# Performance work log

Hardware: AMD Instinct MI355X
Metric: run time of the kernel (lower is better)

Reference implementation:

```python
import jax, jax.numpy as jnp
import numpy as np

N_USERS = 100000
N_ITEMS = 50000
N_NODES = N_USERS + N_ITEMS  # 150000
N_EDGES = 1000000
N_INTENTS = 4
EMBED_K = 64
CHUNK = EMBED_K // N_INTENTS  # 16
N_LAYERS = 3


def setup_inputs() -> dict:
    key = jax.random.key(0)
    k1, k2, k3, k4 = jax.random.split(key, 4)
    Gu = jax.random.normal(k1, (N_USERS, EMBED_K), dtype=jnp.float32) * 0.1
    Gi = jax.random.normal(k2, (N_ITEMS, EMBED_K), dtype=jnp.float32) * 0.1
    edge_index = jax.random.randint(k3, (2, N_EDGES), 0, N_NODES, dtype=jnp.int64)
    edge_index_intents = jax.random.normal(k4, (N_INTENTS, N_EDGES), dtype=jnp.float32)
    return {"Gu": Gu, "Gi": Gi, "edge_index": edge_index,
            "edge_index_intents": edge_index_intents}


def dgcf_layer(x, row, col, edge_index_intents):
    # x: [N, K, C]; edge_index_intents: [K, E]
    w = jax.nn.softmax(edge_index_intents, axis=0).T  # [E, K]
    deg = (jax.ops.segment_sum(w, row, num_segments=N_NODES)
           + jax.ops.segment_sum(w, col, num_segments=N_NODES))  # [N, K]
    # deg^-0.5 with inf -> 0 (as in the torch code)
    dis = jnp.where(deg > 0, 1.0 / jnp.sqrt(jnp.maximum(deg, 1e-12)), 0.0)  # [N, K]
    norm = dis[row] * dis[col]  # [E, K]
    msg = norm[:, :, None] * x[row]  # [E, K, C] gather-multiply
    return jax.ops.segment_sum(msg, col, num_segments=N_NODES)  # scatter-add at targets


def reference(Gu, Gi, edge_index, edge_index_intents):
    row, col = edge_index[0], edge_index[1]
    # ego embeddings split into intent chunks: [N, K, C]
    x = jnp.concatenate([Gu, Gi], axis=0).reshape(N_NODES, N_INTENTS, CHUNK)
    for _ in range(N_LAYERS):
        x = dgcf_layer(x, row, col, edge_index_intents)
    return x
```

## Files before the change

kernel.cpp:

```cpp
#include <hip/hip_runtime.h>
#include <hip/hip_bf16.h>
#include <hip/hip_fp16.h>
#include <math.h>

#define N_USERS 100000
#define N_ITEMS 50000
#define N_NODES 150000
#define N_EDGES 1000000
#define N_GU_FLAT (N_USERS * 64)
#define N_ALL_FLAT (N_NODES * 64)
#define NBUCK 586
#define HPITCH (2 * NBUCK)
#define EPB 4096
#define NEB ((N_EDGES + EPB - 1) / EPB)
#define BCAP 2048
#define FIXS 16777216.0f

typedef __hip_bfloat16 bf16;
typedef unsigned short ushort_t;
typedef unsigned int uint_t;
typedef unsigned long long u64_t;

__device__ __forceinline__ ushort_t f2bs(float f) {
    bf16 h = __float2bfloat16(f);
    return *reinterpret_cast<ushort_t*>(&h);
}
__device__ __forceinline__ float lo2f(uint_t u) {
    float f; *reinterpret_cast<uint_t*>(&f) = u << 16; return f;
}
__device__ __forceinline__ float hi2f(uint_t u) {
    float f; *reinterpret_cast<uint_t*>(&f) = u & 0xFFFF0000u; return f;
}
__device__ __forceinline__ uint_t pack2(float a, float b) {
    return (uint_t)f2bs(a) | ((uint_t)f2bs(b) << 16);
}
__device__ __forceinline__ ushort_t f2hs(float f) {
    __half h = __float2half(f);
    return *reinterpret_cast<ushort_t*>(&h);
}
__device__ __forceinline__ float hs2f(ushort_t u) {
    __half h; *reinterpret_cast<ushort_t*>(&h) = u;
    return __half2float(h);
}
__device__ __forceinline__ int fix24(float w) {
    return (int)__float2int_rn(w * FIXS);
}

__global__ __launch_bounds__(1024) void s1_hist_cast(
        const int* __restrict__ ei,
        const float* __restrict__ Gu, const float* __restrict__ Gi,
        ushort_t* __restrict__ xG, uint_t* __restrict__ H, int gE) {
    int b = blockIdx.x;
    int t = threadIdx.x;
    if (b >= gE) {
        long base = ((long)(b - gE) * 1024 + t) * 4;
        if (base >= N_ALL_FLAT) return;
        float4 v = (base < N_GU_FLAT) ? *(const float4*)(Gu + base)
                                      : *(const float4*)(Gi + (base - N_GU_FLAT));
        uint2 o;
        o.x = pack2(v.x, v.y);
        o.y = pack2(v.z, v.w);
        *(uint2*)(xG + base) = o;
        return;
    }
    __shared__ uint_t h[HPITCH];
    for (int j = t; j < HPITCH; j += 1024) h[j] = 0;
    __syncthreads();
    int eb = b * EPB;
    int lim = min(EPB, N_EDGES - eb);
    for (int i = t; i < lim; i += 1024) {
        int e = eb + i;
        int r = ei[e];
        int c = ei[N_EDGES + e];
        atomicAdd(&h[c >> 8], 1u);
        atomicAdd(&h[NBUCK + (r >> 8)], 1u);
    }
    __syncthreads();
    for (int j = t; j < HPITCH; j += 1024) H[(size_t)b * HPITCH + j] = h[j];
}

__global__ __launch_bounds__(256) void s2a_scan_blocks(
        const uint_t* __restrict__ H, uint_t* __restrict__ bases,
        uint_t* __restrict__ totals) {
    int j = blockIdx.x;
    int t = threadIdx.x;
    __shared__ uint_t s[256];
    uint_t v = (t < NEB) ? H[(size_t)t * HPITCH + j] : 0u;
    s[t] = v;
    __syncthreads();
    for (int off = 1; off < 256; off <<= 1) {
        uint_t a = (t >= off) ? s[t - off] : 0u;
        __syncthreads();
        s[t] += a;
        __syncthreads();
    }
    if (t < NEB) bases[(size_t)t * HPITCH + j] = s[t] - v;
    if (t == 255) totals[j] = s[255];
}

__global__ __launch_bounds__(1024) void s2b_bucket_scan(
        const uint_t* __restrict__ totals,
        uint_t* __restrict__ col_base, uint_t* __restrict__ row_base) {
    __shared__ uint_t s[1024];
    int t = threadIdx.x;
    uint_t v = (t < NBUCK) ? totals[t] : 0u;
    s[t] = v;
    __syncthreads();
    for (int off = 1; off < 1024; off <<= 1) {
        uint_t a = (t >= off) ? s[t - off] : 0u;
        __syncthreads();
        s[t] += a;
        __syncthreads();
    }
    if (t < NBUCK) col_base[t] = s[t] - v;
    if (t == NBUCK - 1) col_base[NBUCK] = s[t];
    __syncthreads();
    uint_t w = (t < NBUCK) ? totals[NBUCK + t] : 0u;
    s[t] = w;
    __syncthreads();
    for (int off = 1; off < 1024; off <<= 1) {
        uint_t a = (t >= off) ? s[t - off] : 0u;
        __syncthreads();
        s[t] += a;
        __syncthreads();
    }
    if (t < NBUCK) row_base[t] = s[t] - w;
    if (t == NBUCK - 1) row_base[NBUCK] = s[t];
}

__global__ __launch_bounds__(1024) void s3_scatter(
        const int* __restrict__ ei, const float* __restrict__ intents,
        const uint_t* __restrict__ bases,
        const uint_t* __restrict__ col_base, const uint_t* __restrict__ row_base,
        uint_t* __restrict__ tmp_meta, u64_t* __restrict__ tmp_w,
        u64_t* __restrict__ tmp_row) {
    extern __shared__ char smem[];
    u64_t*  cw    = (u64_t*)smem;
    u64_t*  rw    = (u64_t*)(smem + 32768);
    uint_t* cmeta = (uint_t*)(smem + 65536);
    uint_t* cpos  = (uint_t*)(smem + 81920);
    uint_t* rpos  = (uint_t*)(smem + 98304);
    uint_t* ctr   = (uint_t*)(smem + 114688);
    uint_t* lexcl = (uint_t*)(smem + 119376);
    uint_t* stmp  = (uint_t*)(smem + 124064);
    int b = blockIdx.x, t = threadIdx.x;
    for (int j = t; j < HPITCH; j += 1024) ctr[j] = 0;
    __syncthreads();
    int eb = b * EPB;
    int lim = min(EPB, N_EDGES - eb);
    int  jcol[4], jrow[4];
    uint_t rkc[4], rkr[4], meta[4];
    u64_t cwv[4], rwv[4];
    bool val[4];
#pragma unroll
    for (int q = 0; q < 4; ++q) {
        int i = t + q * 1024;
        val[q] = (i < lim);
        int e = eb + (val[q] ? i : 0);
        int r = ei[e];
        int c = ei[N_EDGES + e];
        float v0 = intents[e];
        float v1 = intents[N_EDGES + e];
        float v2 = intents[2 * N_EDGES + e];
        float v3 = intents[3 * N_EDGES + e];
        float m  = fmaxf(fmaxf(v0, v1), fmaxf(v2, v3));
        float x0 = __expf(v0 - m), x1 = __expf(v1 - m);
        float x2 = __expf(v2 - m), x3 = __expf(v3 - m);
        float inv = 1.0f / (x0 + x1 + x2 + x3);
        float w0 = x0 * inv, w1 = x1 * inv, w2 = x2 * inv, w3 = x3 * inv;
        jcol[q] = c >> 8;
        jrow[q] = r >> 8;
        if (val[q]) {
            rkc[q] = atomicAdd(&ctr[jcol[q]], 1u);
            rkr[q] = atomicAdd(&ctr[NBUCK + jrow[q]], 1u);
        }
        meta[q] = ((uint_t)(c & 255) << 24) | (uint_t)r;
        cwv[q]  = (u64_t)pack2(w0, w1) | ((u64_t)pack2(w2, w3) << 32);
        rwv[q]  = (u64_t)f2hs(w0) | ((u64_t)f2hs(w1) << 16) |
                  ((u64_t)f2hs(w2) << 32) | ((u64_t)(uint_t)(r & 255) << 48);
    }
    __syncthreads();
    {
        uint_t v = (t < NBUCK) ? ctr[t] : 0u;
        stmp[t] = v;
        __syncthreads();
        for (int off = 1; off < 1024; off <<= 1) {
            uint_t a = (t >= off) ? stmp[t - off] : 0u;
            __syncthreads();
            stmp[t] += a;
            __syncthreads();
        }
        if (t < NBUCK) lexcl[t] = stmp[t] - v;
    }
    __syncthreads();
    {
        uint_t v = (t < NBUCK) ? ctr[NBUCK + t] : 0u;
        stmp[t] = v;
        __syncthreads();
        for (int off = 1; off < 1024; off <<= 1) {
            uint_t a = (t >= off) ? stmp[t - off] : 0u;
            __syncthreads();
            stmp[t] += a;
            __syncthreads();
        }
        if (t < NBUCK) lexcl[NBUCK + t] = stmp[t] - v;
    }
    __syncthreads();
#pragma unroll
    for (int q = 0; q < 4; ++q) {
        if (!val[q]) continue;
        uint_t lp = lexcl[jcol[q]] + rkc[q];
        cmeta[lp] = meta[q];
        cw[lp]    = cwv[q];
        cpos[lp]  = col_base[jcol[q]] + bases[(size_t)b * HPITCH + jcol[q]] + rkc[q];
        uint_t lr = lexcl[NBUCK + jrow[q]] + rkr[q];
        rw[lr]    = rwv[q];
        rpos[lr]  = row_base[jrow[q]] + bases[(size_t)b * HPITCH + NBUCK + jrow[q]] + rkr[q];
    }
    __syncthreads();
    for (int i = t; i < lim; i += 1024) {
        uint_t p = cpos[i];
        tmp_meta[p] = cmeta[i];
        tmp_w[p]    = cw[i];
        tmp_row[rpos[i]] = rw[i];
    }
}

__global__ __launch_bounds__(1024) void s4_finalize(
        const uint_t* __restrict__ tmp_meta, const u64_t* __restrict__ tmp_w,
        const u64_t* __restrict__ tmp_row,
        const uint_t* __restrict__ col_base, const uint_t* __restrict__ row_base,
        uint_t* __restrict__ rec_src, int* __restrict__ offs_c, int* __restrict__ cnt_c,
        float* __restrict__ dis) {
    __shared__ uint_t meta_s[BCAP];
    __shared__ u64_t  w_s[BCAP];
    __shared__ u64_t  rw_s[BCAP];
    __shared__ uint_t hist[256], excl[256], run[256], sc[256];
    __shared__ int deg[1024];
    int b = blockIdx.x, t = threadIdx.x;
    if (t < 256) { hist[t] = 0u; run[t] = 0u; }
    deg[t] = 0;
    __syncthreads();
    uint_t c0 = col_base[b];
    int nc = min((int)(col_base[b + 1] - c0), BCAP);
    uint_t r0 = row_base[b];
    int nr = min((int)(row_base[b + 1] - r0), BCAP);
    for (int i = t; i < nc; i += 1024) {
        meta_s[i] = tmp_meta[c0 + i];
        w_s[i]    = tmp_w[c0 + i];
    }
    for (int i = t; i < nr; i += 1024) rw_s[i] = tmp_row[r0 + i];
    __syncthreads();
    for (int i = t; i < nc; i += 1024) {
        uint_t nl = meta_s[i] >> 24;
        u64_t w = w_s[i];
        atomicAdd(&hist[nl], 1u);
        atomicAdd(&deg[nl * 4 + 0], fix24(lo2f((uint_t)w)));
        atomicAdd(&deg[nl * 4 + 1], fix24(hi2f((uint_t)w)));
        atomicAdd(&deg[nl * 4 + 2], fix24(lo2f((uint_t)(w >> 32))));
        atomicAdd(&deg[nl * 4 + 3], fix24(hi2f((uint_t)(w >> 32))));
    }
    for (int i = t; i < nr; i += 1024) {
        u64_t rv = rw_s[i];
        uint_t nl = (uint_t)(rv >> 48) & 255u;
        float w0 = hs2f((ushort_t)(rv & 0xFFFF));
        float w1 = hs2f((ushort_t)((rv >> 16) & 0xFFFF));
        float w2 = hs2f((ushort_t)((rv >> 32) & 0xFFFF));
        float w3 = 1.0f - w0 - w1 - w2;
        atomicAdd(&deg[nl * 4 + 0], fix24(w0));
        atomicAdd(&deg[nl * 4 + 1], fix24(w1));
        atomicAdd(&deg[nl * 4 + 2], fix24(w2));
        atomicAdd(&deg[nl * 4 + 3], fix24(w3));
    }
    __syncthreads();
    if (t < 256) sc[t] = hist[t];
    __syncthreads();
    for (int off = 1; off < 256; off <<= 1) {
        uint_t a = (t < 256 && t >= off) ? sc[t - off] : 0u;
        __syncthreads();
        if (t < 256) sc[t] += a;
        __syncthreads();
    }
    if (t < 256) excl[t] = sc[t] - hist[t];
    __syncthreads();
    for (int i = t; i < nc; i += 1024) {
        uint_t m = meta_s[i];
        uint_t nl = m >> 24;
        uint_t p = atomicAdd(&run[nl], 1u);
        rec_src[c0 + excl[nl] + p] = m & 0x00FFFFFFu;
    }
    if (t < 256) {
        int n = b * 256 + t;
        if (n < N_NODES) {
            offs_c[n] = (int)(c0 + excl[t]);
            cnt_c[n]  = (int)hist[t];
            float d0 = (float)deg[t * 4 + 0] * (1.0f / FIXS);
            float d1 = (float)deg[t * 4 + 1] * (1.0f / FIXS);
            float d2 = (float)deg[t * 4 + 2] * (1.0f / FIXS);
            float d3 = (float)deg[t * 4 + 3] * (1.0f / FIXS);
            float4 dd;
            dd.x = (d0 > 0.f) ? rsqrtf(fmaxf(d0, 1e-12f)) : 0.f;
            dd.y = (d1 > 0.f) ? rsqrtf(fmaxf(d1, 1e-12f)) : 0.f;
            dd.z = (d2 > 0.f) ? rsqrtf(fmaxf(d2, 1e-12f)) : 0.f;
            dd.w = (d3 > 0.f) ? rsqrtf(fmaxf(d3, 1e-12f)) : 0.f;
            *(float4*)(dis + (size_t)n * 4) = dd;
        }
    }
}

template <int MODE>
__global__ __launch_bounds__(256) void dg_agg(const ushort_t* __restrict__ xin,
                                              ushort_t* __restrict__ xout_b,
                                              float* __restrict__ xout_f,
                                              const uint_t* __restrict__ rec_src,
                                              const int* __restrict__ cnt_c,
                                              const int* __restrict__ offs_c,
                                              const float* __restrict__ dis) {
    int n = (blockIdx.x * 256 + threadIdx.x) >> 3;
    if (n >= N_NODES) return;
    int j = threadIdx.x & 7, k = j >> 1;
    int base = offs_c[n];
    int cnt  = cnt_c[n];
    float dd = dis[n * 4 + k];
    float a0 = 0.f, a1 = 0.f, a2 = 0.f, a3 = 0.f;
    float a4 = 0.f, a5 = 0.f, a6 = 0.f, a7 = 0.f;
    int i = 0;
    for (; i + 2 <= cnt; i += 2) {
        int s0 = (int)rec_src[base + i];
        int s1 = (int)rec_src[base + i + 1];
        uint4 x0 = *(const uint4*)(xin + (long)s0 * 64 + j * 8);
        uint4 x1 = *(const uint4*)(xin + (long)s1 * 64 + j * 8);
        float n0 = 1.f, n1 = 1.f;
        if (MODE == 0) { n0 = dis[s0 * 4 + k]; n1 = dis[s1 * 4 + k]; }
        a0 = fmaf(n0, lo2f(x0.x), a0); a1 = fmaf(n0, hi2f(x0.x), a1);
        a2 = fmaf(n0, lo2f(x0.y), a2); a3 = fmaf(n0, hi2f(x0.y), a3);
        a4 = fmaf(n0, lo2f(x0.z), a4); a5 = fmaf(n0, hi2f(x0.z), a5);
        a6 = fmaf(n0, lo2f(x0.w), a6); a7 = fmaf(n0, hi2f(x0.w), a7);
        a0 = fmaf(n1, lo2f(x1.x), a0); a1 = fmaf(n1, hi2f(x1.x), a1);
        a2 = fmaf(n1, lo2f(x1.y), a2); a3 = fmaf(n1, hi2f(x1.y), a3);
        a4 = fmaf(n1, lo2f(x1.z), a4); a5 = fmaf(n1, hi2f(x1.z), a5);
        a6 = fmaf(n1, lo2f(x1.w), a6); a7 = fmaf(n1, hi2f(x1.w), a7);
    }
    if (i < cnt) {
        int s0 = (int)rec_src[base + i];
        uint4 x0 = *(const uint4*)(xin + (long)s0 * 64 + j * 8);
        float n0 = (MODE == 0) ? dis[s0 * 4 + k] : 1.f;
        a0 = fmaf(n0, lo2f(x0.x), a0); a1 = fmaf(n0, hi2f(x0.x), a1);
        a2 = fmaf(n0, lo2f(x0.y), a2); a3 = fmaf(n0, hi2f(x0.y), a3);
        a4 = fmaf(n0, lo2f(x0.z), a4); a5 = fmaf(n0, hi2f(x0.z), a5);
        a6 = fmaf(n0, lo2f(x0.w), a6); a7 = fmaf(n0, hi2f(x0.w), a7);
    }
    float sc = (MODE == 2) ? dd : dd * dd;
    a0 *= sc; a1 *= sc; a2 *= sc; a3 *= sc;
    a4 *= sc; a5 *= sc; a6 *= sc; a7 *= sc;
    long o = (long)n * 64 + j * 8;
    if (MODE == 2) {
        *(float4*)(xout_f + o)     = make_float4(a0, a1, a2, a3);
        *(float4*)(xout_f + o + 4) = make_float4(a4, a5, a6, a7);
    } else {
        uint4 ob;
        ob.x = pack2(a0, a1); ob.y = pack2(a2, a3);
        ob.z = pack2(a4, a5); ob.w = pack2(a6, a7);
        *(uint4*)(xout_b + o) = ob;
    }
}

extern "C" void kernel_launch(void* const* d_in, const int* in_sizes, int n_in,
                              void* d_out, int out_size, void* d_ws, size_t ws_size,
                              hipStream_t stream) {
    const float* Gu      = (const float*)d_in[0];
    const float* Gi      = (const float*)d_in[1];
    const int*   ei      = (const int*)d_in[2];
    const float* intents = (const float*)d_in[3];
    float* out = (float*)d_out;

    char* ws = (char*)d_ws;
    size_t off = 0;
    int* offs_c = (int*)(ws + off);       off += (size_t)N_NODES * 4;
    int* cnt_c  = (int*)(ws + off);       off += (size_t)N_NODES * 4;
    float* dis  = (float*)(ws + off);     off += (size_t)N_NODES * 16;
    uint_t* rec_src = (uint_t*)(ws + off); off += (size_t)N_EDGES * 4;
    uint_t* col_base = (uint_t*)(ws + off); off += 4096;
    uint_t* row_base = (uint_t*)(ws + off); off += 4096;
    uint_t* totals   = (uint_t*)(ws + off); off += 8192;
    ushort_t* xG = (ushort_t*)(ws + off); off += (size_t)N_ALL_FLAT * 2;
    ushort_t* xA = (ushort_t*)(ws + off); off += (size_t)N_ALL_FLAT * 2;
    ushort_t* xB = (ushort_t*)(ws + off); off += (size_t)N_ALL_FLAT * 2;
    uint_t* tmp_meta = (uint_t*)xA;
    u64_t*  tmp_w    = (u64_t*)((char*)xA + 4000000);
    u64_t*  tmp_row  = (u64_t*)xB;
    uint_t* H     = (uint_t*)((char*)xB + 8000000);
    uint_t* bases = (uint_t*)((char*)xB + 9200000);
    (void)ws_size; (void)in_sizes; (void)n_in; (void)out_size;

    const int gE1 = NEB;
    const int gC1 = (N_ALL_FLAT / 4 + 1023) / 1024;

    s1_hist_cast<<<gE1 + gC1, 1024, 0, stream>>>(ei, Gu, Gi, xG, H, gE1);
    s2a_scan_blocks<<<HPITCH, 256, 0, stream>>>(H, bases, totals);
    s2b_bucket_scan<<<1, 1024, 0, stream>>>(totals, col_base, row_base);

    const size_t S3_LDS = 128160;
    hipFuncSetAttribute((const void*)s3_scatter,
                        hipFuncAttributeMaxDynamicSharedMemorySize, (int)S3_LDS);
    s3_scatter<<<NEB, 1024, S3_LDS, stream>>>(ei, intents, bases, col_base, row_base,
                                              tmp_meta, tmp_w, tmp_row);
    s4_finalize<<<NBUCK, 1024, 0, stream>>>(tmp_meta, tmp_w, tmp_row,
                                            col_base, row_base,
                                            rec_src, offs_c, cnt_c, dis);

    int gAgg = (N_NODES * 8 + 255) / 256;
    dg_agg<0><<<gAgg, 256, 0, stream>>>(xG, xA, nullptr, rec_src, cnt_c, offs_c, dis);
    dg_agg<1><<<gAgg, 256, 0, stream>>>(xA, xB, nullptr, rec_src, cnt_c, offs_c, dis);
    dg_agg<2><<<gAgg, 256, 0, stream>>>(xB, nullptr, out, rec_src, cnt_c, offs_c, dis);
}
```

Measured before the change: 232.3 us.

## Use fixed-capacity bucket slots and cooperative index loading in aggregation

```diff
diff --git a/kernel.cpp b/kernel.cpp
--- a/kernel.cpp
+++ b/kernel.cpp
@@ -79,7 +79,7 @@
     for (int j = t; j < HPITCH; j += 1024) H[(size_t)b * HPITCH + j] = h[j];
 }
 
-__global__ __launch_bounds__(256) void s2a_scan_blocks(
+__global__ __launch_bounds__(256) void s2_scan_blocks(
         const uint_t* __restrict__ H, uint_t* __restrict__ bases,
         uint_t* __restrict__ totals) {
     int j = blockIdx.x;
@@ -98,40 +98,9 @@
     if (t == 255) totals[j] = s[255];
 }
 
-__global__ __launch_bounds__(1024) void s2b_bucket_scan(
-        const uint_t* __restrict__ totals,
-        uint_t* __restrict__ col_base, uint_t* __restrict__ row_base) {
-    __shared__ uint_t s[1024];
-    int t = threadIdx.x;
-    uint_t v = (t < NBUCK) ? totals[t] : 0u;
-    s[t] = v;
-    __syncthreads();
-    for (int off = 1; off < 1024; off <<= 1) {
-        uint_t a = (t >= off) ? s[t - off] : 0u;
-        __syncthreads();
-        s[t] += a;
-        __syncthreads();
-    }
-    if (t < NBUCK) col_base[t] = s[t] - v;
-    if (t == NBUCK - 1) col_base[NBUCK] = s[t];
-    __syncthreads();
-    uint_t w = (t < NBUCK) ? totals[NBUCK + t] : 0u;
-    s[t] = w;
-    __syncthreads();
-    for (int off = 1; off < 1024; off <<= 1) {
-        uint_t a = (t >= off) ? s[t - off] : 0u;
-        __syncthreads();
-        s[t] += a;
-        __syncthreads();
-    }
-    if (t < NBUCK) row_base[t] = s[t] - w;
-    if (t == NBUCK - 1) row_base[NBUCK] = s[t];
-}
-
 __global__ __launch_bounds__(1024) void s3_scatter(
         const int* __restrict__ ei, const float* __restrict__ intents,
         const uint_t* __restrict__ bases,
-        const uint_t* __restrict__ col_base, const uint_t* __restrict__ row_base,
         uint_t* __restrict__ tmp_meta, u64_t* __restrict__ tmp_w,
         u64_t* __restrict__ tmp_row) {
     extern __shared__ char smem[];
@@ -212,10 +181,10 @@
         uint_t lp = lexcl[jcol[q]] + rkc[q];
         cmeta[lp] = meta[q];
         cw[lp]    = cwv[q];
-        cpos[lp]  = col_base[jcol[q]] + bases[(size_t)b * HPITCH + jcol[q]] + rkc[q];
+        cpos[lp]  = (uint_t)jcol[q] * BCAP + bases[(size_t)b * HPITCH + jcol[q]] + rkc[q];
         uint_t lr = lexcl[NBUCK + jrow[q]] + rkr[q];
         rw[lr]    = rwv[q];
-        rpos[lr]  = row_base[jrow[q]] + bases[(size_t)b * HPITCH + NBUCK + jrow[q]] + rkr[q];
+        rpos[lr]  = (uint_t)jrow[q] * BCAP + bases[(size_t)b * HPITCH + NBUCK + jrow[q]] + rkr[q];
     }
     __syncthreads();
     for (int i = t; i < lim; i += 1024) {
@@ -228,8 +197,7 @@
 
 __global__ __launch_bounds__(1024) void s4_finalize(
         const uint_t* __restrict__ tmp_meta, const u64_t* __restrict__ tmp_w,
-        const u64_t* __restrict__ tmp_row,
-        const uint_t* __restrict__ col_base, const uint_t* __restrict__ row_base,
+        const u64_t* __restrict__ tmp_row, const uint_t* __restrict__ totals,
         uint_t* __restrict__ rec_src, int* __restrict__ offs_c, int* __restrict__ cnt_c,
         float* __restrict__ dis) {
     __shared__ uint_t meta_s[BCAP];
@@ -241,15 +209,14 @@
     if (t < 256) { hist[t] = 0u; run[t] = 0u; }
     deg[t] = 0;
     __syncthreads();
-    uint_t c0 = col_base[b];
-    int nc = min((int)(col_base[b + 1] - c0), BCAP);
-    uint_t r0 = row_base[b];
-    int nr = min((int)(row_base[b + 1] - r0), BCAP);
+    uint_t c0 = (uint_t)b * BCAP;
+    int nc = min((int)totals[b], BCAP);
+    int nr = min((int)totals[NBUCK + b], BCAP);
     for (int i = t; i < nc; i += 1024) {
         meta_s[i] = tmp_meta[c0 + i];
         w_s[i]    = tmp_w[c0 + i];
     }
-    for (int i = t; i < nr; i += 1024) rw_s[i] = tmp_row[r0 + i];
+    for (int i = t; i < nr; i += 1024) rw_s[i] = tmp_row[c0 + i];
     __syncthreads();
     for (int i = t; i < nc; i += 1024) {
         uint_t nl = meta_s[i] >> 24;
@@ -318,37 +285,31 @@
                                               const float* __restrict__ dis) {
     int n = (blockIdx.x * 256 + threadIdx.x) >> 3;
     if (n >= N_NODES) return;
-    int j = threadIdx.x & 7, k = j >> 1;
+    int lane = threadIdx.x & 63;
+    int j = lane & 7, k = j >> 1;
+    int sg = lane & 56;
     int base = offs_c[n];
     int cnt  = cnt_c[n];
     float dd = dis[n * 4 + k];
     float a0 = 0.f, a1 = 0.f, a2 = 0.f, a3 = 0.f;
     float a4 = 0.f, a5 = 0.f, a6 = 0.f, a7 = 0.f;
-    int i = 0;
-    for (; i + 2 <= cnt; i += 2) {
-        int s0 = (int)rec_src[base + i];
-        int s1 = (int)rec_src[base + i + 1];
-        uint4 x0 = *(const uint4*)(xin + (long)s0 * 64 + j * 8);
-        uint4 x1 = *(const uint4*)(xin + (long)s1 * 64 + j * 8);
-        float n0 = 1.f, n1 = 1.f;
-        if (MODE == 0) { n0 = dis[s0 * 4 + k]; n1 = dis[s1 * 4 + k]; }
-        a0 = fmaf(n0, lo2f(x0.x), a0); a1 = fmaf(n0, hi2f(x0.x), a1);
-        a2 = fmaf(n0, lo2f(x0.y), a2); a3 = fmaf(n0, hi2f(x0.y), a3);
-        a4 = fmaf(n0, lo2f(x0.z), a4); a5 = fmaf(n0, hi2f(x0.z), a5);
-        a6 = fmaf(n0, lo2f(x0.w), a6); a7 = fmaf(n0, hi2f(x0.w), a7);
-        a0 = fmaf(n1, lo2f(x1.x), a0); a1 = fmaf(n1, hi2f(x1.x), a1);
-        a2 = fmaf(n1, lo2f(x1.y), a2); a3 = fmaf(n1, hi2f(x1.y), a3);
-        a4 = fmaf(n1, lo2f(x1.z), a4); a5 = fmaf(n1, hi2f(x1.z), a5);
-        a6 = fmaf(n1, lo2f(x1.w), a6); a7 = fmaf(n1, hi2f(x1.w), a7);
-    }
-    if (i < cnt) {
-        int s0 = (int)rec_src[base + i];
-        uint4 x0 = *(const uint4*)(xin + (long)s0 * 64 + j * 8);
-        float n0 = (MODE == 0) ? dis[s0 * 4 + k] : 1.f;
-        a0 = fmaf(n0, lo2f(x0.x), a0); a1 = fmaf(n0, hi2f(x0.x), a1);
-        a2 = fmaf(n0, lo2f(x0.y), a2); a3 = fmaf(n0, hi2f(x0.y), a3);
-        a4 = fmaf(n0, lo2f(x0.z), a4); a5 = fmaf(n0, hi2f(x0.z), a5);
-        a6 = fmaf(n0, lo2f(x0.w), a6); a7 = fmaf(n0, hi2f(x0.w), a7);
+    for (int c = 0; c < cnt; c += 8) {
+        int idx = c + j;
+        uint_t sv = (idx < cnt) ? rec_src[base + idx] : 0u;
+        int srcs[8];
+#pragma unroll
+        for (int i = 0; i < 8; ++i) srcs[i] = (int)__shfl(sv, sg + i, 64);
+#pragma unroll
+        for (int i = 0; i < 8; ++i) {
+            bool v = (c + i) < cnt;
+            int src = v ? srcs[i] : srcs[0];
+            float nk = v ? ((MODE == 0) ? dis[src * 4 + k] : 1.f) : 0.f;
+            uint4 xu = *(const uint4*)(xin + (long)src * 64 + j * 8);
+            a0 = fmaf(nk, lo2f(xu.x), a0); a1 = fmaf(nk, hi2f(xu.x), a1);
+            a2 = fmaf(nk, lo2f(xu.y), a2); a3 = fmaf(nk, hi2f(xu.y), a3);
+            a4 = fmaf(nk, lo2f(xu.z), a4); a5 = fmaf(nk, hi2f(xu.z), a5);
+            a6 = fmaf(nk, lo2f(xu.w), a6); a7 = fmaf(nk, hi2f(xu.w), a7);
+        }
     }
     float sc = (MODE == 2) ? dd : dd * dd;
     a0 *= sc; a1 *= sc; a2 *= sc; a3 *= sc;
@@ -379,34 +340,30 @@
     int* offs_c = (int*)(ws + off);       off += (size_t)N_NODES * 4;
     int* cnt_c  = (int*)(ws + off);       off += (size_t)N_NODES * 4;
     float* dis  = (float*)(ws + off);     off += (size_t)N_NODES * 16;
-    uint_t* rec_src = (uint_t*)(ws + off); off += (size_t)N_EDGES * 4;
-    uint_t* col_base = (uint_t*)(ws + off); off += 4096;
-    uint_t* row_base = (uint_t*)(ws + off); off += 4096;
+    uint_t* rec_src = (uint_t*)(ws + off); off += (size_t)NBUCK * BCAP * 4;
     uint_t* totals   = (uint_t*)(ws + off); off += 8192;
     ushort_t* xG = (ushort_t*)(ws + off); off += (size_t)N_ALL_FLAT * 2;
     ushort_t* xA = (ushort_t*)(ws + off); off += (size_t)N_ALL_FLAT * 2;
     ushort_t* xB = (ushort_t*)(ws + off); off += (size_t)N_ALL_FLAT * 2;
     uint_t* tmp_meta = (uint_t*)xA;
-    u64_t*  tmp_w    = (u64_t*)((char*)xA + 4000000);
+    u64_t*  tmp_w    = (u64_t*)((char*)xA + (size_t)NBUCK * BCAP * 4);
     u64_t*  tmp_row  = (u64_t*)xB;
-    uint_t* H     = (uint_t*)((char*)xB + 8000000);
-    uint_t* bases = (uint_t*)((char*)xB + 9200000);
+    uint_t* H     = (uint_t*)((char*)xB + (size_t)NBUCK * BCAP * 8);
+    uint_t* bases = (uint_t*)((char*)xB + (size_t)NBUCK * BCAP * 8 + 1200000);
     (void)ws_size; (void)in_sizes; (void)n_in; (void)out_size;
 
     const int gE1 = NEB;
     const int gC1 = (N_ALL_FLAT / 4 + 1023) / 1024;
 
     s1_hist_cast<<<gE1 + gC1, 1024, 0, stream>>>(ei, Gu, Gi, xG, H, gE1);
-    s2a_scan_blocks<<<HPITCH, 256, 0, stream>>>(H, bases, totals);
-    s2b_bucket_scan<<<1, 1024, 0, stream>>>(totals, col_base, row_base);
+    s2_scan_blocks<<<HPITCH, 256, 0, stream>>>(H, bases, totals);
 
     const size_t S3_LDS = 128160;
     hipFuncSetAttribute((const void*)s3_scatter,
                         hipFuncAttributeMaxDynamicSharedMemorySize, (int)S3_LDS);
-    s3_scatter<<<NEB, 1024, S3_LDS, stream>>>(ei, intents, bases, col_base, row_base,
+    s3_scatter<<<NEB, 1024, S3_LDS, stream>>>(ei, intents, bases,
                                               tmp_meta, tmp_w, tmp_row);
-    s4_finalize<<<NBUCK, 1024, 0, stream>>>(tmp_meta, tmp_w, tmp_row,
-                                            col_base, row_base,
+    s4_finalize<<<NBUCK, 1024, 0, stream>>>(tmp_meta, tmp_w, tmp_row, totals,
                                             rec_src, offs_c, cnt_c, dis);
 
     int gAgg = (N_NODES * 8 + 255) / 256;
```

After: 224.3 us. 1.04x faster.
